# Performance work log

Measured on AMD Instinct MI355X. Metric: run time of the kernel, lower is better.

## Reference

```python
import jax, jax.numpy as jnp
import numpy as np

N_NODES = 50000
FEAT_DIM = 64
N_PAIRS = 400000  # symmetrized -> 800000 directed edges
NUM_ITERATIONS = 8
ALPHA = 0.9
BETA = 0.5
MAX_HOPS = 6  # fixed bound replacing the data-dependent BFS while-loop
INF = 1e9


def setup_inputs() -> dict:
    key = jax.random.key(0)
    k1, k2, k3, k4 = jax.random.split(key, 4)
    x = jax.random.normal(k1, (N_NODES, FEAT_DIM), dtype=jnp.float32)
    src = jax.random.randint(k2, (N_PAIRS,), 0, N_NODES, dtype=jnp.int32)
    dst = jax.random.randint(k3, (N_PAIRS,), 0, N_NODES, dtype=jnp.int32)
    # undirected graph: include both edge directions, as PyG datasets do
    edge_index = jnp.stack([jnp.concatenate([src, dst]), jnp.concatenate([dst, src])])
    mask = jax.random.uniform(k4, (N_NODES, FEAT_DIM)) < 0.02
    return {"x": x, "edge_index": edge_index, "mask": mask}


def _pcfi_forward(x, edge_index, mask):
    N, F = x.shape
    row, col = edge_index[0], edge_index[1]
    # --- compute_f_n2d (feature-wise branch): per-channel BFS hop distance ---
    # dist[f, n] = hop distance of node n from the observed set of channel f.
    dist0 = jnp.where(mask.T, 0.0, INF).astype(jnp.float32)  # [F, N]

    def hop(d, _):
        cand = jax.vmap(lambda dd: jax.ops.segment_min(dd[row] + 1.0, col, num_segments=N))(d)
        return jnp.minimum(d, cand), None

    dist, _ = jax.lax.scan(hop, dist0, None, length=MAX_HOPS)
    # nodes never reached keep 0, matching the torch zeros-init of f_n2d
    f_n2d = jnp.where(dist >= INF * 0.5, 0.0, dist)  # [F, N]

    # --- compute_edge_weight_c per channel: w = alpha^(d_col - d_row + 1), row-degree normalized ---
    w = ALPHA ** (f_n2d[:, col] - f_n2d[:, row] + 1.0)  # [F, E]
    deg = jax.vmap(lambda ww: jax.ops.segment_sum(ww, row, num_segments=N))(w)  # [F, N]
    deg_inv = jnp.where(deg > 0, 1.0 / deg, 0.0)  # inf -> 0 as in masked_fill_
    A = w * deg_inv[:, row]  # [F, E] normalized sparse adjacency values per channel

    # --- iterative propagation with masked reset (all channels batched) ---
    xt, mt = x.T, mask.T  # [F, N]
    out = jnp.where(mt, xt, 0.0)

    def step(o, _):
        # sparse mm: out_new[row] = sum_e A[e] * out[col[e]]
        o = jax.vmap(lambda a, oo: jax.ops.segment_sum(a * oo[col], row, num_segments=N))(A, o)
        return jnp.where(mt, xt, o), None

    out, _ = jax.lax.scan(step, out, None, length=NUM_ITERATIONS)

    # --- correlation-weighted residual fusion ---
    cor = jnp.nan_to_num(jnp.corrcoef(out))  # [F, F]; rows of `out` are the channel variables
    cor = cor * (1.0 - jnp.eye(F, dtype=cor.dtype))  # fill_diagonal_(0)
    out_nf = out.T  # [N, F]
    fT = f_n2d.T  # [N, F]
    a1 = (ALPHA ** fT) * (out_nf - jnp.mean(out_nf, axis=0))
    a2 = a1 @ cor
    return out_nf + BETA * (1.0 - ALPHA ** fT) * a2


def reference(x, edge_index, mask):
    return _pcfi_forward(x, edge_index, mask)
```

## Files before the change

kernel.cpp:

```cpp
#include <hip/hip_runtime.h>
#include <stdint.h>

__device__ __constant__ float c_tab[16] = {
  1.6935087808430286f, 1.5241579027587256f, 1.3717421124828532f,
  1.2345679012345678f, 1.1111111111111112f, 1.0f, 0.9f, 0.81f,
  0.729f, 0.6561f, 0.59049f, 0.531441f, 0.4782969f, 0.43046721f,
  0.387420489f, 0.3486784401f };

__device__ __forceinline__ float bf2f(uint32_t u) {
  union { unsigned int i; float f; } v; v.i = u << 16; return v.f;
}
__device__ __forceinline__ uint16_t f2bf(float f) {
  union { float f; unsigned int i; } v; v.f = f;
  unsigned r = v.i + 0x7FFFu + ((v.i >> 16) & 1u);
  return (uint16_t)(r >> 16);
}

__global__ void k_detect(const uint8_t* __restrict__ m, int nbytes,
                         int* __restrict__ flag) {
  int i = blockIdx.x * blockDim.x + threadIdx.x;
  if (i < nbytes && (i & 3) && m[i]) atomicOr(flag, 1);
}

__global__ void k_init_masks(const uint8_t* __restrict__ raw,
                             const int* __restrict__ flag,
                             unsigned long long* __restrict__ R, int N) {
  int n = blockIdx.x * blockDim.x + threadIdx.x;
  if (n >= N) return;
  unsigned long long r = 0;
  if (*flag) {
    const unsigned long long* m8 =
        (const unsigned long long*)(raw + (size_t)n * 64);
#pragma unroll
    for (int q = 0; q < 8; ++q) {
      unsigned long long v = m8[q] & 0x0101010101010101ULL;
      unsigned long long byte = (v * 0x0102040810204080ULL) >> 56;
      r |= byte << (8 * q);
    }
  } else {
    const int* mi = (const int*)raw + (size_t)n * 64;
#pragma unroll
    for (int f = 0; f < 64; ++f)
      if (mi[f]) r |= 1ULL << f;
  }
  R[n] = r;
}

__global__ void k_bfs_pull(const int* __restrict__ row_ptr,
                           const uint16_t* __restrict__ dst_csr,
                           const unsigned long long* __restrict__ Rold,
                           unsigned long long* __restrict__ Rnew, int N) {
  int n = blockIdx.x * blockDim.x + threadIdx.x;
  if (n >= N) return;
  unsigned long long r = Rold[n];
  if (r == ~0ULL) { Rnew[n] = r; return; }
  int s = row_ptr[n], s1 = row_ptr[n + 1];
  for (; s + 8 <= s1; s += 8) {
    int d0 = dst_csr[s], d1 = dst_csr[s+1], d2 = dst_csr[s+2], d3 = dst_csr[s+3];
    int d4 = dst_csr[s+4], d5 = dst_csr[s+5], d6 = dst_csr[s+6], d7 = dst_csr[s+7];
    unsigned long long r0 = Rold[d0] | Rold[d1];
    unsigned long long r1 = Rold[d2] | Rold[d3];
    unsigned long long r2 = Rold[d4] | Rold[d5];
    unsigned long long r3 = Rold[d6] | Rold[d7];
    r |= (r0 | r1) | (r2 | r3);
  }
  for (; s < s1; ++s) r |= Rold[dst_csr[s]];
  Rnew[n] = r;
}

__global__ void k_distpw_z(const unsigned long long* __restrict__ R,
                           const float* __restrict__ x,
                           uint16_t* __restrict__ pwq, uint16_t* __restrict__ zq,
                           int N) {
  int wave = (blockIdx.x * blockDim.x + threadIdx.x) >> 6;
  int lane = threadIdx.x & 63;
  if (wave >= N) return;
  int d = 0;
#pragma unroll
  for (int h = 0; h < 6; ++h)
    d += (int)((~R[(size_t)h * N + wave] >> lane) & 1ULL);
  if (!((R[(size_t)6 * N + wave] >> lane) & 1ULL)) d = 0;
  float p = c_tab[d + 5];
  size_t ni = (size_t)wave * 64 + lane;
  pwq[ni] = f2bf(p);
  bool obs = (R[wave] >> lane) & 1ULL;
  zq[ni] = obs ? f2bf(p * x[ni]) : (uint16_t)0;
}

__global__ void k_count(const int* __restrict__ row, int* __restrict__ cnt, int E) {
  int e = blockIdx.x * blockDim.x + threadIdx.x;
  if (e < E) atomicAdd(&cnt[row[e]], 1);
}

__global__ void k_bsum(const int* __restrict__ cnt, int* __restrict__ bsum, int N) {
  __shared__ int sm[256];
  int b = blockIdx.x, t = threadIdx.x;
  int i = b * 256 + t;
  int v = (i < N) ? cnt[i] : 0;
  sm[t] = v;
  __syncthreads();
  for (int off = 128; off > 0; off >>= 1) {
    if (t < off) sm[t] += sm[t + off];
    __syncthreads();
  }
  if (t == 0) bsum[b] = sm[0];
}

__global__ void k_bscan(const int* __restrict__ bsum, int* __restrict__ ebsum,
                        int* __restrict__ row_ptr_N, int NB) {
  __shared__ int sm[256];
  int t = threadIdx.x;
  int v = (t < NB) ? bsum[t] : 0;
  sm[t] = v;
  __syncthreads();
  for (int off = 1; off < 256; off <<= 1) {
    int tv = (t >= off) ? sm[t - off] : 0;
    __syncthreads();
    sm[t] += tv;
    __syncthreads();
  }
  if (t < NB) ebsum[t] = sm[t] - v;
  if (t == 255) *row_ptr_N = sm[255];
}

__global__ void k_chscan(const int* __restrict__ cnt, const int* __restrict__ ebsum,
                         int* __restrict__ row_ptr, int* __restrict__ bcur, int N) {
  __shared__ int sm[256];
  int b = blockIdx.x, t = threadIdx.x;
  int i = b * 256 + t;
  int v = (i < N) ? cnt[i] : 0;
  sm[t] = v;
  __syncthreads();
  for (int off = 1; off < 256; off <<= 1) {
    int tv = (t >= off) ? sm[t - off] : 0;
    __syncthreads();
    sm[t] += tv;
    __syncthreads();
  }
  if (i < N) {
    int ex = ebsum[b] + sm[t] - v;
    row_ptr[i] = ex;
    if (t == 0) bcur[b] = ex;
  }
}

__global__ void k_bucket(const int* __restrict__ row, const int* __restrict__ col,
                         int* __restrict__ bcur, uint32_t* __restrict__ staged,
                         int E, int NBUK) {
  __shared__ int cntb[256];
  __shared__ int offb[256];
  int t = threadIdx.x;
  cntb[t] = 0;
  __syncthreads();
  int base = blockIdx.x * 4096;
#pragma unroll
  for (int k = 0; k < 16; ++k) {
    int e = base + k * 256 + t;
    if (e < E) atomicAdd(&cntb[row[e] >> 8], 1);
  }
  __syncthreads();
  {
    int c = cntb[t];
    offb[t] = (t < NBUK && c) ? atomicAdd(&bcur[t], c) : 0;
    cntb[t] = 0;
  }
  __syncthreads();
#pragma unroll
  for (int k = 0; k < 16; ++k) {
    int e = base + k * 256 + t;
    if (e < E) {
      int r = row[e], b = r >> 8;
      int pos = offb[b] + atomicAdd(&cntb[b], 1);
      staged[pos] = ((uint32_t)(r & 255) << 16) | (uint32_t)col[e];
    }
  }
}

__global__ void k_unbucket(const int* __restrict__ row_ptr,
                           const uint32_t* __restrict__ staged,
                           uint16_t* __restrict__ dst_csr, int N) {
  __shared__ int curs[256];
  int b = blockIdx.x, t = threadIdx.x;
  int nb = b * 256;
  int rlast = min(nb + 256, N);
  if (nb + t < rlast) curs[t] = row_ptr[nb + t];
  __syncthreads();
  int start = row_ptr[nb], end = row_ptr[rlast];
  for (int i = start + t; i < end; i += 256) {
    uint32_t v = staged[i];
    int pos = atomicAdd(&curs[v >> 16], 1);
    dst_csr[pos] = (uint16_t)(v & 0xFFFF);
  }
}


#define ACC8(v0, v1)                                              \
  a0 += bf2f(v0.x & 0xFFFF) + bf2f(v1.x & 0xFFFF);                \
  a1 += bf2f(v0.x >> 16)    + bf2f(v1.x >> 16);                   \
  a2 += bf2f(v0.y & 0xFFFF) + bf2f(v1.y & 0xFFFF);                \
  a3 += bf2f(v0.y >> 16)    + bf2f(v1.y >> 16);                   \
  a4 += bf2f(v0.z & 0xFFFF) + bf2f(v1.z & 0xFFFF);                \
  a5 += bf2f(v0.z >> 16)    + bf2f(v1.z >> 16);                   \
  a6 += bf2f(v0.w & 0xFFFF) + bf2f(v1.w & 0xFFFF);                \
  a7 += bf2f(v0.w >> 16)    + bf2f(v1.w >> 16);

#define ACC8_1(v)                                                 \
  a0 += bf2f(v.x & 0xFFFF); a1 += bf2f(v.x >> 16);                \
  a2 += bf2f(v.y & 0xFFFF); a3 += bf2f(v.y >> 16);                \
  a4 += bf2f(v.z & 0xFFFF); a5 += bf2f(v.z >> 16);                \
  a6 += bf2f(v.w & 0xFFFF); a7 += bf2f(v.w >> 16);

#define RED8()                                                    \
  a0 += __shfl_xor(a0, 8); a0 += __shfl_xor(a0, 16); a0 += __shfl_xor(a0, 32); \
  a1 += __shfl_xor(a1, 8); a1 += __shfl_xor(a1, 16); a1 += __shfl_xor(a1, 32); \
  a2 += __shfl_xor(a2, 8); a2 += __shfl_xor(a2, 16); a2 += __shfl_xor(a2, 32); \
  a3 += __shfl_xor(a3, 8); a3 += __shfl_xor(a3, 16); a3 += __shfl_xor(a3, 32); \
  a4 += __shfl_xor(a4, 8); a4 += __shfl_xor(a4, 16); a4 += __shfl_xor(a4, 32); \
  a5 += __shfl_xor(a5, 8); a5 += __shfl_xor(a5, 16); a5 += __shfl_xor(a5, 32); \
  a6 += __shfl_xor(a6, 8); a6 += __shfl_xor(a6, 16); a6 += __shfl_xor(a6, 32); \
  a7 += __shfl_xor(a7, 8); a7 += __shfl_xor(a7, 16); a7 += __shfl_xor(a7, 32);

__global__ void k_sinv_g(const int* __restrict__ row_ptr, const uint16_t* __restrict__ dst_csr,
                         const uint4* __restrict__ pwq4, float* __restrict__ sinv,
                         uint4* __restrict__ gq4, int N) {
  int wave = (blockIdx.x * blockDim.x + threadIdx.x) >> 6;
  int lane = threadIdx.x & 63;
  if (wave >= N) return;
  int g = lane >> 3, cq = lane & 7;
  int base = row_ptr[wave], s1 = row_ptr[wave + 1];
  int nfull = (s1 - base) >> 4;
  float a0 = 0.f, a1 = 0.f, a2 = 0.f, a3 = 0.f, a4 = 0.f, a5 = 0.f, a6 = 0.f, a7 = 0.f;
  int s = base + g;
  for (int it = 0; it < nfull; ++it, s += 16) {
    int d0 = dst_csr[s], d1 = dst_csr[s + 8];
    uint4 v0 = pwq4[(size_t)d0 * 8 + cq];
    uint4 v1 = pwq4[(size_t)d1 * 8 + cq];
    ACC8(v0, v1)
  }
  for (s = base + (nfull << 4) + g; s < s1; s += 8) {
    uint4 v = pwq4[(size_t)dst_csr[s] * 8 + cq];
    ACC8_1(v)
  }
  RED8()
  if (g == 0) {
    float s0 = (a0 > 0.f) ? (1.f / a0) : 0.f;
    float s1f = (a1 > 0.f) ? (1.f / a1) : 0.f;
    float s2 = (a2 > 0.f) ? (1.f / a2) : 0.f;
    float s3 = (a3 > 0.f) ? (1.f / a3) : 0.f;
    float s4 = (a4 > 0.f) ? (1.f / a4) : 0.f;
    float s5 = (a5 > 0.f) ? (1.f / a5) : 0.f;
    float s6 = (a6 > 0.f) ? (1.f / a6) : 0.f;
    float s7 = (a7 > 0.f) ? (1.f / a7) : 0.f;
    size_t b64 = (size_t)wave * 64 + (cq << 3);
    *(float4*)(sinv + b64) = make_float4(s0, s1f, s2, s3);
    *(float4*)(sinv + b64 + 4) = make_float4(s4, s5, s6, s7);
    uint4 pv = pwq4[(size_t)wave * 8 + cq];
    uint32_t g0 = f2bf(bf2f(pv.x & 0xFFFF) * s0);
    uint32_t g1 = f2bf(bf2f(pv.x >> 16) * s1f);
    uint32_t g2 = f2bf(bf2f(pv.y & 0xFFFF) * s2);
    uint32_t g3 = f2bf(bf2f(pv.y >> 16) * s3);
    uint32_t g4 = f2bf(bf2f(pv.z & 0xFFFF) * s4);
    uint32_t g5 = f2bf(bf2f(pv.z >> 16) * s5);
    uint32_t g6 = f2bf(bf2f(pv.w & 0xFFFF) * s6);
    uint32_t g7 = f2bf(bf2f(pv.w >> 16) * s7);
    uint4 gw;
    gw.x = g0 | (g1 << 16); gw.y = g2 | (g3 << 16);
    gw.z = g4 | (g5 << 16); gw.w = g6 | (g7 << 16);
    gq4[(size_t)wave * 8 + cq] = gw;
  }
}

__global__ void k_prop_q(const int* __restrict__ row_ptr, const uint16_t* __restrict__ dst_csr,
                         const uint4* __restrict__ gq4,
                         const unsigned long long* __restrict__ R0,
                         const uint4* __restrict__ zprev4,
                         uint4* __restrict__ znew4, int N) {
  int wave = (blockIdx.x * blockDim.x + threadIdx.x) >> 6;
  int lane = threadIdx.x & 63;
  if (wave >= N) return;
  int g = lane >> 3, cq = lane & 7;
  int base = row_ptr[wave], s1 = row_ptr[wave + 1];
  int nfull = (s1 - base) >> 4;
  float a0 = 0.f, a1 = 0.f, a2 = 0.f, a3 = 0.f, a4 = 0.f, a5 = 0.f, a6 = 0.f, a7 = 0.f;
  int s = base + g;
  for (int it = 0; it < nfull; ++it, s += 16) {
    int d0 = dst_csr[s], d1 = dst_csr[s + 8];
    uint4 v0 = zprev4[(size_t)d0 * 8 + cq];
    uint4 v1 = zprev4[(size_t)d1 * 8 + cq];
    ACC8(v0, v1)
  }
  for (s = base + (nfull << 4) + g; s < s1; s += 8) {
    uint4 v = zprev4[(size_t)dst_csr[s] * 8 + cq];
    ACC8_1(v)
  }
  RED8()
  if (g == 0) {
    size_t bidx = (size_t)wave * 8 + cq;
    uint4 gv = gq4[bidx];
    uint4 zp = zprev4[bidx];
    unsigned long long r0 = R0[wave];
    int c0 = cq << 3;
    uint32_t n0 = ((r0 >> c0) & 1ULL)       ? (zp.x & 0xFFFF) : (uint32_t)f2bf(bf2f(gv.x & 0xFFFF) * a0);
    uint32_t n1 = ((r0 >> (c0 + 1)) & 1ULL) ? (zp.x >> 16)    : (uint32_t)f2bf(bf2f(gv.x >> 16) * a1);
    uint32_t n2 = ((r0 >> (c0 + 2)) & 1ULL) ? (zp.y & 0xFFFF) : (uint32_t)f2bf(bf2f(gv.y & 0xFFFF) * a2);
    uint32_t n3 = ((r0 >> (c0 + 3)) & 1ULL) ? (zp.y >> 16)    : (uint32_t)f2bf(bf2f(gv.y >> 16) * a3);
    uint32_t n4 = ((r0 >> (c0 + 4)) & 1ULL) ? (zp.z & 0xFFFF) : (uint32_t)f2bf(bf2f(gv.z & 0xFFFF) * a4);
    uint32_t n5 = ((r0 >> (c0 + 5)) & 1ULL) ? (zp.z >> 16)    : (uint32_t)f2bf(bf2f(gv.z >> 16) * a5);
    uint32_t n6 = ((r0 >> (c0 + 6)) & 1ULL) ? (zp.w & 0xFFFF) : (uint32_t)f2bf(bf2f(gv.w & 0xFFFF) * a6);
    uint32_t n7 = ((r0 >> (c0 + 7)) & 1ULL) ? (zp.w >> 16)    : (uint32_t)f2bf(bf2f(gv.w >> 16) * a7);
    uint4 outw;
    outw.x = n0 | (n1 << 16); outw.y = n2 | (n3 << 16);
    outw.z = n4 | (n5 << 16); outw.w = n6 | (n7 << 16);
    znew4[bidx] = outw;
  }
}

__global__ void k_prop_final(const int* __restrict__ row_ptr, const uint16_t* __restrict__ dst_csr,
                             const float* __restrict__ sinv,
                             const unsigned long long* __restrict__ R0,
                             const float* __restrict__ x,
                             const uint4* __restrict__ zprev4,
                             float* __restrict__ o, int N) {
  int wave = (blockIdx.x * blockDim.x + threadIdx.x) >> 6;
  int lane = threadIdx.x & 63;
  if (wave >= N) return;
  int g = lane >> 3, cq = lane & 7;
  int base = row_ptr[wave], s1 = row_ptr[wave + 1];
  int nfull = (s1 - base) >> 4;
  float a0 = 0.f, a1 = 0.f, a2 = 0.f, a3 = 0.f, a4 = 0.f, a5 = 0.f, a6 = 0.f, a7 = 0.f;
  int s = base + g;
  for (int it = 0; it < nfull; ++it, s += 16) {
    int d0 = dst_csr[s], d1 = dst_csr[s + 8];
    uint4 v0 = zprev4[(size_t)d0 * 8 + cq];
    uint4 v1 = zprev4[(size_t)d1 * 8 + cq];
    ACC8(v0, v1)
  }
  for (s = base + (nfull << 4) + g; s < s1; s += 8) {
    uint4 v = zprev4[(size_t)dst_csr[s] * 8 + cq];
    ACC8_1(v)
  }
  RED8()
  if (g == 0) {
    size_t b64 = (size_t)wave * 64 + (cq << 3);
    float4 svA = *(const float4*)(sinv + b64);
    float4 svB = *(const float4*)(sinv + b64 + 4);
    float4 xvA = *(const float4*)(x + b64);
    float4 xvB = *(const float4*)(x + b64 + 4);
    unsigned long long r0 = R0[wave];
    int c0 = cq << 3;
    float o0 = ((r0 >> c0) & 1ULL)       ? xvA.x : svA.x * a0;
    float o1 = ((r0 >> (c0 + 1)) & 1ULL) ? xvA.y : svA.y * a1;
    float o2 = ((r0 >> (c0 + 2)) & 1ULL) ? xvA.z : svA.z * a2;
    float o3 = ((r0 >> (c0 + 3)) & 1ULL) ? xvA.w : svA.w * a3;
    float o4 = ((r0 >> (c0 + 4)) & 1ULL) ? xvB.x : svB.x * a4;
    float o5 = ((r0 >> (c0 + 5)) & 1ULL) ? xvB.y : svB.y * a5;
    float o6 = ((r0 >> (c0 + 6)) & 1ULL) ? xvB.z : svB.z * a6;
    float o7 = ((r0 >> (c0 + 7)) & 1ULL) ? xvB.w : svB.w * a7;
    *(float4*)(o + b64) = make_float4(o0, o1, o2, o3);
    *(float4*)(o + b64 + 4) = make_float4(o4, o5, o6, o7);
  }
}

__global__ void k_covar(const float* __restrict__ o, float* __restrict__ Cpart,
                        float* __restrict__ mupart, int N) {
  __shared__ float yt[32][68];
  __shared__ float ms[64];
  int t = threadIdx.x, blk = blockIdx.x;
  if (t < 64) ms[t] = 0.f;
  int i0 = (t >> 4) * 4, j0 = (t & 15) * 4;
  float acc[4][4] = {};
  float csum = 0.f;
  for (size_t base = (size_t)blk * 32; base < (size_t)N;
       base += (size_t)gridDim.x * 32) {
    int rows = min(32, N - (int)base);
    for (int k = t; k < rows * 64; k += 256) {
      int nn = k >> 6, f = k & 63;
      float val = o[(base + nn) * 64 + f];
      yt[nn][f] = val;
      csum += val;
    }
    __syncthreads();
    for (int nn = 0; nn < rows; ++nn) {
      float4 a = *(const float4*)&yt[nn][i0];
      float4 b = *(const float4*)&yt[nn][j0];
      acc[0][0] += a.x * b.x; acc[0][1] += a.x * b.y; acc[0][2] += a.x * b.z; acc[0][3] += a.x * b.w;
      acc[1][0] += a.y * b.x; acc[1][1] += a.y * b.y; acc[1][2] += a.y * b.z; acc[1][3] += a.y * b.w;
      acc[2][0] += a.z * b.x; acc[2][1] += a.z * b.y; acc[2][2] += a.z * b.z; acc[2][3] += a.z * b.w;
      acc[3][0] += a.w * b.x; acc[3][1] += a.w * b.y; acc[3][2] += a.w * b.z; acc[3][3] += a.w * b.w;
    }
    __syncthreads();
  }
  float* Cb = Cpart + (size_t)blk * 4096;
#pragma unroll
  for (int a = 0; a < 4; ++a)
#pragma unroll
    for (int b = 0; b < 4; ++b)
      Cb[(size_t)(i0 + a) * 64 + j0 + b] = acc[a][b];
  atomicAdd(&ms[t & 63], csum);
  __syncthreads();
  if (t < 64) mupart[(size_t)blk * 64 + t] = ms[t];
}

__global__ void k_redC(const float* __restrict__ Cpart, float* __restrict__ M2,
                       int NBLK) {
  __shared__ float sm[16][17];
  int t = threadIdx.x;
  int li = t >> 4, part = t & 15;
  int idx = blockIdx.x * 16 + li;
  int per = NBLK >> 4;
  float s = 0.f;
  int b0 = part * per;
  for (int b = b0; b < b0 + per; ++b)
    s += Cpart[(size_t)b * 4096 + idx];
  sm[li][part] = s;
  __syncthreads();
  if (part == 0) {
    float tot = 0.f;
#pragma unroll
    for (int k = 0; k < 16; ++k) tot += sm[li][k];
    M2[idx] = tot;
  }
}

__global__ void k_redMu(const float* __restrict__ mupart, float* __restrict__ musum,
                        int NBLK) {
  int t = blockIdx.x * blockDim.x + threadIdx.x;
  int idx = t >> 4, part = t & 15;
  if (idx >= 64) return;
  int per = NBLK >> 4;
  float s = 0.f;
  int b0 = part * per;
  for (int b = b0; b < b0 + per; ++b)
    s += mupart[(size_t)b * 64 + idx];
  atomicAdd(&musum[idx], s);
}

__global__ void k_cor(const float* __restrict__ M2, const float* __restrict__ musum,
                      float* __restrict__ cor, int N) {
  int idx = blockIdx.x * blockDim.x + threadIdx.x;
  if (idx >= 4096) return;
  int i = idx >> 6, j = idx & 63;
  float inv_n = 1.f / (float)N;
  float mi = musum[i] * inv_n, mj = musum[j] * inv_n;
  float Cij = M2[idx] - (float)N * mi * mj;
  float Cii = M2[i * 64 + i] - (float)N * mi * mi;
  float Cjj = M2[j * 64 + j] - (float)N * mj * mj;
  float d = sqrtf(Cii * Cjj);
  cor[idx] = (i != j && d > 0.f) ? (Cij / d) : 0.f;
}

__global__ void k_fuse2(float* o, const uint16_t* __restrict__ pwq,
                        const float* __restrict__ musum, const float* __restrict__ cor,
                        int N) {
  __shared__ float a1t[64][65];
  __shared__ float scor[64][65];
  __shared__ float smu[64];
  int t = threadIdx.x;
  int nbase = blockIdx.x * 64;
  if (t < 64) smu[t] = musum[t] / (float)N;
#pragma unroll
  for (int j = 0; j < 16; ++j) {
    int idx = t + 256 * j;
    scor[idx >> 6][idx & 63] = cor[idx];
  }
  __syncthreads();
#pragma unroll
  for (int j = 0; j < 16; ++j) {
    int idx = t + 256 * j;
    int r = idx >> 6, c = idx & 63;
    int n = nbase + r;
    float val = 0.f;
    if (n < N) {
      size_t gidx = (size_t)n * 64 + c;
      val = bf2f(pwq[gidx]) * (o[gidx] - smu[c]);
    }
    a1t[r][c] = val;
  }
  __syncthreads();
  int tr = (t >> 4) * 4, tc = (t & 15) * 4;
  float acc[4][4] = {};
  for (int k = 0; k < 64; ++k) {
    float a[4], b[4];
#pragma unroll
    for (int i = 0; i < 4; ++i) a[i] = a1t[tr + i][k];
#pragma unroll
    for (int j = 0; j < 4; ++j) b[j] = scor[k][tc + j];
#pragma unroll
    for (int i = 0; i < 4; ++i)
#pragma unroll
      for (int j = 0; j < 4; ++j) acc[i][j] += a[i] * b[j];
  }
#pragma unroll
  for (int i = 0; i < 4; ++i) {
    int n = nbase + tr + i;
    if (n < N) {
#pragma unroll
      for (int j = 0; j < 4; ++j) {
        size_t gidx = (size_t)n * 64 + tc + j;
        float p = bf2f(pwq[gidx]);
        o[gidx] = o[gidx] + 0.5f * (1.f - p) * acc[i][j];
      }
    }
  }
}

extern "C" void kernel_launch(void* const* d_in, const int* in_sizes, int n_in,
                              void* d_out, int out_size, void* d_ws, size_t ws_size,
                              hipStream_t stream) {
  const float* x = (const float*)d_in[0];
  const int* ei = (const int*)d_in[1];
  const uint8_t* mask_raw = (const uint8_t*)d_in[2];
  int N = in_sizes[0] / 64;
  int E = in_sizes[1] / 2;
  const int* row = ei;
  const int* col = ei + E;

  char* w = (char*)d_ws;
  size_t off = 0;
  auto alloc = [&](size_t bytes) -> void* {
    void* p = w + off;
    off += (bytes + 255) & ~(size_t)255;
    return p;
  };
  unsigned long long* R = (unsigned long long*)alloc((size_t)7 * N * 8);
  int* dflag = (int*)alloc(256);
  int* cnt = (int*)alloc((size_t)N * 4);
  int* row_ptr = (int*)alloc((size_t)(N + 1) * 4);
  uint16_t* dst_csr = (uint16_t*)alloc((size_t)E * 2);
  uint32_t* staged = (uint32_t*)alloc((size_t)E * 4);
  int* bcur = (int*)alloc(256 * 4);
  int* bsum = (int*)alloc(256 * 4);
  int* ebsum = (int*)alloc(256 * 4);
  uint16_t* pwq = (uint16_t*)alloc((size_t)N * 64 * 2);
  float* sinv = (float*)alloc((size_t)N * 64 * 4);
  uint16_t* gq = (uint16_t*)alloc((size_t)N * 64 * 2);
  uint16_t* zqA = (uint16_t*)alloc((size_t)N * 64 * 2);
  uint16_t* zqB = (uint16_t*)alloc((size_t)N * 64 * 2);
  const int CVB = 256;
  float* Cpart = (float*)alloc((size_t)CVB * 4096 * 4);
  float* mupart = (float*)alloc((size_t)CVB * 64 * 4);
  float* M2 = (float*)alloc(4096 * 4);
  float* musum = (float*)alloc(256);
  float* cor = (float*)alloc(4096 * 4);
  float* o = (float*)d_out;

  int gN = (N + 255) / 256;
  int gE = (E + 255) / 256;
  int total = N * 64;
  int gT = (total + 255) / 256;
  int NB = (N + 255) / 256;
  int NBUK = (N + 255) / 256;
  int gBK = (E + 4095) / 4096;

  hipMemsetAsync(dflag, 0, 4, stream);
  k_detect<<<gT, 256, 0, stream>>>(mask_raw, total, dflag);
  k_init_masks<<<gN, 256, 0, stream>>>(mask_raw, dflag, R, N);

  hipMemsetAsync(cnt, 0, (size_t)N * 4, stream);
  k_count<<<gE, 256, 0, stream>>>(row, cnt, E);
  k_bsum<<<NB, 256, 0, stream>>>(cnt, bsum, N);
  k_bscan<<<1, 256, 0, stream>>>(bsum, ebsum, row_ptr + N, NB);
  k_chscan<<<NB, 256, 0, stream>>>(cnt, ebsum, row_ptr, bcur, N);
  k_bucket<<<gBK, 256, 0, stream>>>(row, col, bcur, staged, E, NBUK);
  k_unbucket<<<NBUK, 256, 0, stream>>>(row_ptr, staged, dst_csr, N);

  for (int h = 0; h < 6; ++h)
    k_bfs_pull<<<gN, 256, 0, stream>>>(row_ptr, dst_csr, R + (size_t)h * N,
                                       R + (size_t)(h + 1) * N, N);
  k_distpw_z<<<gT, 256, 0, stream>>>(R, x, pwq, zqA, N);

  k_sinv_g<<<gT, 256, 0, stream>>>(row_ptr, dst_csr, (const uint4*)pwq, sinv,
                                   (uint4*)gq, N);

  uint16_t* zsrc = zqA;
  uint16_t* zdst = zqB;
  for (int it = 0; it < 7; ++it) {
    k_prop_q<<<gT, 256, 0, stream>>>(row_ptr, dst_csr, (const uint4*)gq, R,
                                     (const uint4*)zsrc, (uint4*)zdst, N);
    uint16_t* tmp = zsrc; zsrc = zdst; zdst = tmp;
  }
  k_prop_final<<<gT, 256, 0, stream>>>(row_ptr, dst_csr, sinv, R, x,
                                       (const uint4*)zsrc, o, N);

  k_covar<<<CVB, 256, 0, stream>>>(o, Cpart, mupart, N);
  hipMemsetAsync(musum, 0, 256, stream);
  k_redC<<<256, 256, 0, stream>>>(Cpart, M2, CVB);
  k_redMu<<<4, 256, 0, stream>>>(mupart, musum, CVB);
  k_cor<<<16, 256, 0, stream>>>(M2, musum, cor, N);

  int gF = (N + 63) / 64;
  k_fuse2<<<gF, 256, 0, stream>>>(o, pwq, musum, cor, N);
}
```

Baseline: 421.1 us.

## Split bf16 feature arrays into two 32-channel halves for SpMM gathers

Stores the bf16 propagation state and power weights as two planes of 32 channels each, instead of one interleaved 64-channel array. Each SpMM wave now handles one node-half, with 16 edge groups of 4 lanes instead of 8 groups of 8 lanes. Blocks are interleaved so both halves of the same nodes run close together in time. The intent is to shrink each half's gather working set so it fits better in cache and to fetch more neighbours in parallel per wave, at the cost of reading the edge list twice, doubling the wave count and adding an extra shuffle stage.

```diff
diff --git a/kernel.cpp b/kernel.cpp
--- a/kernel.cpp
+++ b/kernel.cpp
@@ -70,7 +70,7 @@
 
 __global__ void k_distpw_z(const unsigned long long* __restrict__ R,
                            const float* __restrict__ x,
-                           uint16_t* __restrict__ pwq, uint16_t* __restrict__ zq,
+                           uint16_t* __restrict__ pwq_s, uint16_t* __restrict__ zq_s,
                            int N) {
   int wave = (blockIdx.x * blockDim.x + threadIdx.x) >> 6;
   int lane = threadIdx.x & 63;
@@ -81,10 +81,11 @@
     d += (int)((~R[(size_t)h * N + wave] >> lane) & 1ULL);
   if (!((R[(size_t)6 * N + wave] >> lane) & 1ULL)) d = 0;
   float p = c_tab[d + 5];
-  size_t ni = (size_t)wave * 64 + lane;
-  pwq[ni] = f2bf(p);
+  int half = lane >> 5, c = lane & 31;
+  size_t si = (size_t)half * N * 32 + (size_t)wave * 32 + c;
+  pwq_s[si] = f2bf(p);
   bool obs = (R[wave] >> lane) & 1ULL;
-  zq[ni] = obs ? f2bf(p * x[ni]) : (uint16_t)0;
+  zq_s[si] = obs ? f2bf(p * x[(size_t)wave * 64 + lane]) : (uint16_t)0;
 }
 
 __global__ void k_count(const int* __restrict__ row, int* __restrict__ cnt, int E) {
@@ -210,38 +211,46 @@
   a4 += bf2f(v.z & 0xFFFF); a5 += bf2f(v.z >> 16);                \
   a6 += bf2f(v.w & 0xFFFF); a7 += bf2f(v.w >> 16);
 
-#define RED8()                                                    \
-  a0 += __shfl_xor(a0, 8); a0 += __shfl_xor(a0, 16); a0 += __shfl_xor(a0, 32); \
-  a1 += __shfl_xor(a1, 8); a1 += __shfl_xor(a1, 16); a1 += __shfl_xor(a1, 32); \
-  a2 += __shfl_xor(a2, 8); a2 += __shfl_xor(a2, 16); a2 += __shfl_xor(a2, 32); \
-  a3 += __shfl_xor(a3, 8); a3 += __shfl_xor(a3, 16); a3 += __shfl_xor(a3, 32); \
-  a4 += __shfl_xor(a4, 8); a4 += __shfl_xor(a4, 16); a4 += __shfl_xor(a4, 32); \
-  a5 += __shfl_xor(a5, 8); a5 += __shfl_xor(a5, 16); a5 += __shfl_xor(a5, 32); \
-  a6 += __shfl_xor(a6, 8); a6 += __shfl_xor(a6, 16); a6 += __shfl_xor(a6, 32); \
-  a7 += __shfl_xor(a7, 8); a7 += __shfl_xor(a7, 16); a7 += __shfl_xor(a7, 32);
+#define RED8S()                                                                 \
+  a0 += __shfl_xor(a0, 4); a0 += __shfl_xor(a0, 8); a0 += __shfl_xor(a0, 16); a0 += __shfl_xor(a0, 32); \
+  a1 += __shfl_xor(a1, 4); a1 += __shfl_xor(a1, 8); a1 += __shfl_xor(a1, 16); a1 += __shfl_xor(a1, 32); \
+  a2 += __shfl_xor(a2, 4); a2 += __shfl_xor(a2, 8); a2 += __shfl_xor(a2, 16); a2 += __shfl_xor(a2, 32); \
+  a3 += __shfl_xor(a3, 4); a3 += __shfl_xor(a3, 8); a3 += __shfl_xor(a3, 16); a3 += __shfl_xor(a3, 32); \
+  a4 += __shfl_xor(a4, 4); a4 += __shfl_xor(a4, 8); a4 += __shfl_xor(a4, 16); a4 += __shfl_xor(a4, 32); \
+  a5 += __shfl_xor(a5, 4); a5 += __shfl_xor(a5, 8); a5 += __shfl_xor(a5, 16); a5 += __shfl_xor(a5, 32); \
+  a6 += __shfl_xor(a6, 4); a6 += __shfl_xor(a6, 8); a6 += __shfl_xor(a6, 16); a6 += __shfl_xor(a6, 32); \
+  a7 += __shfl_xor(a7, 4); a7 += __shfl_xor(a7, 8); a7 += __shfl_xor(a7, 16); a7 += __shfl_xor(a7, 32);
+
+#define SPLIT_HEAD(N)                                             \
+  int bid = blockIdx.x;                                           \
+  int half = (bid & 7) >> 2;                                      \
+  int idx = (bid >> 3) * 4 + (bid & 3);                           \
+  int node = idx * 4 + (int)(threadIdx.x >> 6);                   \
+  if (node >= (N)) return;                                        \
+  int lane = threadIdx.x & 63;                                    \
+  int cq = lane & 3, g = lane >> 2;
 
 __global__ void k_sinv_g(const int* __restrict__ row_ptr, const uint16_t* __restrict__ dst_csr,
-                         const uint4* __restrict__ pwq4, float* __restrict__ sinv,
-                         uint4* __restrict__ gq4, int N) {
-  int wave = (blockIdx.x * blockDim.x + threadIdx.x) >> 6;
-  int lane = threadIdx.x & 63;
-  if (wave >= N) return;
-  int g = lane >> 3, cq = lane & 7;
-  int base = row_ptr[wave], s1 = row_ptr[wave + 1];
-  int nfull = (s1 - base) >> 4;
+                         const uint16_t* __restrict__ pwq_s, float* __restrict__ sinv,
+                         uint16_t* __restrict__ gq_s, int N) {
+  SPLIT_HEAD(N)
+  const uint4* pw4 = (const uint4*)(pwq_s + (size_t)half * N * 32);
+  uint4* gq4 = (uint4*)(gq_s + (size_t)half * N * 32);
+  int base = row_ptr[node], s1 = row_ptr[node + 1];
+  int nfull = (s1 - base) >> 5;
   float a0 = 0.f, a1 = 0.f, a2 = 0.f, a3 = 0.f, a4 = 0.f, a5 = 0.f, a6 = 0.f, a7 = 0.f;
   int s = base + g;
-  for (int it = 0; it < nfull; ++it, s += 16) {
-    int d0 = dst_csr[s], d1 = dst_csr[s + 8];
-    uint4 v0 = pwq4[(size_t)d0 * 8 + cq];
-    uint4 v1 = pwq4[(size_t)d1 * 8 + cq];
+  for (int it = 0; it < nfull; ++it, s += 32) {
+    int d0 = dst_csr[s], d1 = dst_csr[s + 16];
+    uint4 v0 = pw4[(size_t)d0 * 4 + cq];
+    uint4 v1 = pw4[(size_t)d1 * 4 + cq];
     ACC8(v0, v1)
   }
-  for (s = base + (nfull << 4) + g; s < s1; s += 8) {
-    uint4 v = pwq4[(size_t)dst_csr[s] * 8 + cq];
+  for (s = base + (nfull << 5) + g; s < s1; s += 16) {
+    uint4 v = pw4[(size_t)dst_csr[s] * 4 + cq];
     ACC8_1(v)
   }
-  RED8()
+  RED8S()
   if (g == 0) {
     float s0 = (a0 > 0.f) ? (1.f / a0) : 0.f;
     float s1f = (a1 > 0.f) ? (1.f / a1) : 0.f;
@@ -251,10 +260,10 @@
     float s5 = (a5 > 0.f) ? (1.f / a5) : 0.f;
     float s6 = (a6 > 0.f) ? (1.f / a6) : 0.f;
     float s7 = (a7 > 0.f) ? (1.f / a7) : 0.f;
-    size_t b64 = (size_t)wave * 64 + (cq << 3);
+    size_t b64 = (size_t)node * 64 + half * 32 + (cq << 3);
     *(float4*)(sinv + b64) = make_float4(s0, s1f, s2, s3);
     *(float4*)(sinv + b64 + 4) = make_float4(s4, s5, s6, s7);
-    uint4 pv = pwq4[(size_t)wave * 8 + cq];
+    uint4 pv = pw4[(size_t)node * 4 + cq];
     uint32_t g0 = f2bf(bf2f(pv.x & 0xFFFF) * s0);
     uint32_t g1 = f2bf(bf2f(pv.x >> 16) * s1f);
     uint32_t g2 = f2bf(bf2f(pv.y & 0xFFFF) * s2);
@@ -266,40 +275,40 @@
     uint4 gw;
     gw.x = g0 | (g1 << 16); gw.y = g2 | (g3 << 16);
     gw.z = g4 | (g5 << 16); gw.w = g6 | (g7 << 16);
-    gq4[(size_t)wave * 8 + cq] = gw;
+    gq4[(size_t)node * 4 + cq] = gw;
   }
 }
 
 __global__ void k_prop_q(const int* __restrict__ row_ptr, const uint16_t* __restrict__ dst_csr,
-                         const uint4* __restrict__ gq4,
+                         const uint16_t* __restrict__ gq_s,
                          const unsigned long long* __restrict__ R0,
-                         const uint4* __restrict__ zprev4,
-                         uint4* __restrict__ znew4, int N) {
-  int wave = (blockIdx.x * blockDim.x + threadIdx.x) >> 6;
-  int lane = threadIdx.x & 63;
-  if (wave >= N) return;
-  int g = lane >> 3, cq = lane & 7;
-  int base = row_ptr[wave], s1 = row_ptr[wave + 1];
-  int nfull = (s1 - base) >> 4;
+                         const uint16_t* __restrict__ zprev_s,
+                         uint16_t* __restrict__ znew_s, int N) {
+  SPLIT_HEAD(N)
+  const uint4* z4 = (const uint4*)(zprev_s + (size_t)half * N * 32);
+  const uint4* gq4 = (const uint4*)(gq_s + (size_t)half * N * 32);
+  uint4* zn4 = (uint4*)(znew_s + (size_t)half * N * 32);
+  int base = row_ptr[node], s1 = row_ptr[node + 1];
+  int nfull = (s1 - base) >> 5;
   float a0 = 0.f, a1 = 0.f, a2 = 0.f, a3 = 0.f, a4 = 0.f, a5 = 0.f, a6 = 0.f, a7 = 0.f;
   int s = base + g;
-  for (int it = 0; it < nfull; ++it, s += 16) {
-    int d0 = dst_csr[s], d1 = dst_csr[s + 8];
-    uint4 v0 = zprev4[(size_t)d0 * 8 + cq];
-    uint4 v1 = zprev4[(size_t)d1 * 8 + cq];
+  for (int it = 0; it < nfull; ++it, s += 32) {
+    int d0 = dst_csr[s], d1 = dst_csr[s + 16];
+    uint4 v0 = z4[(size_t)d0 * 4 + cq];
+    uint4 v1 = z4[(size_t)d1 * 4 + cq];
     ACC8(v0, v1)
   }
-  for (s = base + (nfull << 4) + g; s < s1; s += 8) {
-    uint4 v = zprev4[(size_t)dst_csr[s] * 8 + cq];
+  for (s = base + (nfull << 5) + g; s < s1; s += 16) {
+    uint4 v = z4[(size_t)dst_csr[s] * 4 + cq];
     ACC8_1(v)
   }
-  RED8()
+  RED8S()
   if (g == 0) {
-    size_t bidx = (size_t)wave * 8 + cq;
+    size_t bidx = (size_t)node * 4 + cq;
     uint4 gv = gq4[bidx];
-    uint4 zp = zprev4[bidx];
-    unsigned long long r0 = R0[wave];
-    int c0 = cq << 3;
+    uint4 zp = z4[bidx];
+    unsigned long long r0 = R0[node];
+    int c0 = half * 32 + (cq << 3);
     uint32_t n0 = ((r0 >> c0) & 1ULL)       ? (zp.x & 0xFFFF) : (uint32_t)f2bf(bf2f(gv.x & 0xFFFF) * a0);
     uint32_t n1 = ((r0 >> (c0 + 1)) & 1ULL) ? (zp.x >> 16)    : (uint32_t)f2bf(bf2f(gv.x >> 16) * a1);
     uint32_t n2 = ((r0 >> (c0 + 2)) & 1ULL) ? (zp.y & 0xFFFF) : (uint32_t)f2bf(bf2f(gv.y & 0xFFFF) * a2);
@@ -311,7 +320,7 @@
     uint4 outw;
     outw.x = n0 | (n1 << 16); outw.y = n2 | (n3 << 16);
     outw.z = n4 | (n5 << 16); outw.w = n6 | (n7 << 16);
-    znew4[bidx] = outw;
+    zn4[bidx] = outw;
   }
 }
 
@@ -319,35 +328,33 @@
                              const float* __restrict__ sinv,
                              const unsigned long long* __restrict__ R0,
                              const float* __restrict__ x,
-                             const uint4* __restrict__ zprev4,
+                             const uint16_t* __restrict__ zprev_s,
                              float* __restrict__ o, int N) {
-  int wave = (blockIdx.x * blockDim.x + threadIdx.x) >> 6;
-  int lane = threadIdx.x & 63;
-  if (wave >= N) return;
-  int g = lane >> 3, cq = lane & 7;
-  int base = row_ptr[wave], s1 = row_ptr[wave + 1];
-  int nfull = (s1 - base) >> 4;
+  SPLIT_HEAD(N)
+  const uint4* z4 = (const uint4*)(zprev_s + (size_t)half * N * 32);
+  int base = row_ptr[node], s1 = row_ptr[node + 1];
+  int nfull = (s1 - base) >> 5;
   float a0 = 0.f, a1 = 0.f, a2 = 0.f, a3 = 0.f, a4 = 0.f, a5 = 0.f, a6 = 0.f, a7 = 0.f;
   int s = base + g;
-  for (int it = 0; it < nfull; ++it, s += 16) {
-    int d0 = dst_csr[s], d1 = dst_csr[s + 8];
-    uint4 v0 = zprev4[(size_t)d0 * 8 + cq];
-    uint4 v1 = zprev4[(size_t)d1 * 8 + cq];
+  for (int it = 0; it < nfull; ++it, s += 32) {
+    int d0 = dst_csr[s], d1 = dst_csr[s + 16];
+    uint4 v0 = z4[(size_t)d0 * 4 + cq];
+    uint4 v1 = z4[(size_t)d1 * 4 + cq];
     ACC8(v0, v1)
   }
-  for (s = base + (nfull << 4) + g; s < s1; s += 8) {
-    uint4 v = zprev4[(size_t)dst_csr[s] * 8 + cq];
+  for (s = base + (nfull << 5) + g; s < s1; s += 16) {
+    uint4 v = z4[(size_t)dst_csr[s] * 4 + cq];
     ACC8_1(v)
   }
-  RED8()
+  RED8S()
   if (g == 0) {
-    size_t b64 = (size_t)wave * 64 + (cq << 3);
+    size_t b64 = (size_t)node * 64 + half * 32 + (cq << 3);
     float4 svA = *(const float4*)(sinv + b64);
     float4 svB = *(const float4*)(sinv + b64 + 4);
     float4 xvA = *(const float4*)(x + b64);
     float4 xvB = *(const float4*)(x + b64 + 4);
-    unsigned long long r0 = R0[wave];
-    int c0 = cq << 3;
+    unsigned long long r0 = R0[node];
+    int c0 = half * 32 + (cq << 3);
     float o0 = ((r0 >> c0) & 1ULL)       ? xvA.x : svA.x * a0;
     float o1 = ((r0 >> (c0 + 1)) & 1ULL) ? xvA.y : svA.y * a1;
     float o2 = ((r0 >> (c0 + 2)) & 1ULL) ? xvA.z : svA.z * a2;
@@ -449,7 +456,7 @@
   cor[idx] = (i != j && d > 0.f) ? (Cij / d) : 0.f;
 }
 
-__global__ void k_fuse2(float* o, const uint16_t* __restrict__ pwq,
+__global__ void k_fuse2(float* o, const uint16_t* __restrict__ pwq_s,
                         const float* __restrict__ musum, const float* __restrict__ cor,
                         int N) {
   __shared__ float a1t[64][65];
@@ -471,8 +478,8 @@
     int n = nbase + r;
     float val = 0.f;
     if (n < N) {
-      size_t gidx = (size_t)n * 64 + c;
-      val = bf2f(pwq[gidx]) * (o[gidx] - smu[c]);
+      size_t pidx = (size_t)(c >> 5) * N * 32 + (size_t)n * 32 + (c & 31);
+      val = bf2f(pwq_s[pidx]) * (o[(size_t)n * 64 + c] - smu[c]);
     }
     a1t[r][c] = val;
   }
@@ -496,8 +503,10 @@
     if (n < N) {
 #pragma unroll
       for (int j = 0; j < 4; ++j) {
-        size_t gidx = (size_t)n * 64 + tc + j;
-        float p = bf2f(pwq[gidx]);
+        int c = tc + j;
+        size_t pidx = (size_t)(c >> 5) * N * 32 + (size_t)n * 32 + (c & 31);
+        float p = bf2f(pwq_s[pidx]);
+        size_t gidx = (size_t)n * 64 + c;
         o[gidx] = o[gidx] + 0.5f * (1.f - p) * acc[i][j];
       }
     }
@@ -551,6 +560,8 @@
   int NB = (N + 255) / 256;
   int NBUK = (N + 255) / 256;
   int gBK = (E + 4095) / 4096;
+  int nodeBlocks = (N + 3) / 4;
+  int gS = ((nodeBlocks * 2 + 7) / 8) * 8;
 
   hipMemsetAsync(dflag, 0, 4, stream);
   k_detect<<<gT, 256, 0, stream>>>(mask_raw, total, dflag);
@@ -569,18 +580,15 @@
                                        R + (size_t)(h + 1) * N, N);
   k_distpw_z<<<gT, 256, 0, stream>>>(R, x, pwq, zqA, N);
 
-  k_sinv_g<<<gT, 256, 0, stream>>>(row_ptr, dst_csr, (const uint4*)pwq, sinv,
-                                   (uint4*)gq, N);
+  k_sinv_g<<<gS, 256, 0, stream>>>(row_ptr, dst_csr, pwq, sinv, gq, N);
 
   uint16_t* zsrc = zqA;
   uint16_t* zdst = zqB;
   for (int it = 0; it < 7; ++it) {
-    k_prop_q<<<gT, 256, 0, stream>>>(row_ptr, dst_csr, (const uint4*)gq, R,
-                                     (const uint4*)zsrc, (uint4*)zdst, N);
+    k_prop_q<<<gS, 256, 0, stream>>>(row_ptr, dst_csr, gq, R, zsrc, zdst, N);
     uint16_t* tmp = zsrc; zsrc = zdst; zdst = tmp;
   }
-  k_prop_final<<<gT, 256, 0, stream>>>(row_ptr, dst_csr, sinv, R, x,
-                                       (const uint4*)zsrc, o, N);
+  k_prop_final<<<gS, 256, 0, stream>>>(row_ptr, dst_csr, sinv, R, x, zsrc, o, N);
 
   k_covar<<<CVB, 256, 0, stream>>>(o, Cpart, mupart, N);
   hipMemsetAsync(musum, 0, 256, stream);
```

Result: slower. 566.5 us (+34.5%).
